# Kernel tuning notes

Hardware: AMD Instinct MI355X
Metric: run time of the kernel (lower is better)

The kernel has to match this reference:

```python
import jax, jax.numpy as jnp
import numpy as np

B_SZ = 1
SEQ = 4096
IN_DIM = 1024
D_MODEL = 512
D_INNER = 1024   # expand(2) * d_model
D_STATE = 16
D_CONV = 4
DT_RANK = 32     # ceil(d_model / 16)
N_LAYERS = 2
N_CLASSES = 2


def setup_inputs() -> dict:
    key = jax.random.key(0)
    ks = jax.random.split(key, 12)
    s = 0.02
    x = jax.random.normal(ks[0], (B_SZ, SEQ, IN_DIM), jnp.float32)
    fc1_w = jax.random.normal(ks[1], (D_MODEL, IN_DIM), jnp.float32) * s
    fc1_b = jnp.zeros((D_MODEL,), jnp.float32)
    ln_w = jnp.ones((N_LAYERS, D_MODEL), jnp.float32)
    ln_b = jnp.zeros((N_LAYERS, D_MODEL), jnp.float32)
    in_proj_w = jax.random.normal(ks[2], (N_LAYERS, 2 * D_INNER, D_MODEL), jnp.float32) * s
    conv_w = jax.random.normal(ks[3], (N_LAYERS, D_INNER, D_CONV), jnp.float32) * 0.1
    conv_b = jnp.zeros((N_LAYERS, D_INNER), jnp.float32)
    x_proj_w = jax.random.normal(ks[4], (N_LAYERS, DT_RANK + 2 * D_STATE, D_INNER), jnp.float32) * s
    dt_proj_w = jax.random.normal(ks[5], (N_LAYERS, D_INNER, DT_RANK), jnp.float32) * s
    # bias so softplus(bias) ~ 0.01 (typical dt init)
    dt_proj_b = jnp.full((N_LAYERS, D_INNER), float(np.log(np.expm1(0.01))), jnp.float32)
    A_log = jnp.broadcast_to(jnp.log(jnp.arange(1, D_STATE + 1, dtype=jnp.float32)),
                             (N_LAYERS, D_INNER, D_STATE)).copy()
    D_skip = jnp.ones((N_LAYERS, D_INNER), jnp.float32)
    norm_w = jnp.ones((D_MODEL,), jnp.float32)
    norm_b = jnp.zeros((D_MODEL,), jnp.float32)
    cls_w = jax.random.normal(ks[6], (N_CLASSES, D_MODEL), jnp.float32) * s
    cls_b = jnp.zeros((N_CLASSES,), jnp.float32)
    return {"x": x, "fc1_w": fc1_w, "fc1_b": fc1_b, "ln_w": ln_w, "ln_b": ln_b,
            "in_proj_w": in_proj_w, "conv_w": conv_w, "conv_b": conv_b,
            "x_proj_w": x_proj_w, "dt_proj_w": dt_proj_w, "dt_proj_b": dt_proj_b,
            "A_log": A_log, "D_skip": D_skip, "norm_w": norm_w, "norm_b": norm_b,
            "cls_w": cls_w, "cls_b": cls_b}


def layernorm(h, w, b, eps=1e-5):
    mu = h.mean(-1, keepdims=True)
    var = ((h - mu) ** 2).mean(-1, keepdims=True)
    return (h - mu) * jax.lax.rsqrt(var + eps) * w + b


def mamba_block(h, in_proj_w, conv_w, conv_b, x_proj_w, dt_proj_w, dt_proj_b, A_log, D_skip):
    # h: [B, L, d_model]
    xz = jnp.einsum('bld,ed->ble', h, in_proj_w)          # [B, L, 2*D_INNER]
    xc, z = jnp.split(xz, 2, axis=-1)                     # each [B, L, D_INNER]
    # causal depthwise conv along L (kernel D_CONV)
    xp = jnp.pad(xc, ((0, 0), (D_CONV - 1, 0), (0, 0)))
    conv = sum(xp[:, k:k + xc.shape[1], :] * conv_w[:, k] for k in range(D_CONV))
    xc = jax.nn.silu(conv + conv_b)
    dbc = jnp.einsum('bld,ed->ble', xc, x_proj_w)         # [B, L, DT_RANK + 2*N]
    dt = jax.nn.softplus(jnp.einsum('blr,dr->bld', dbc[..., :DT_RANK], dt_proj_w) + dt_proj_b)
    Bm = dbc[..., DT_RANK:DT_RANK + D_STATE]              # [B, L, N]
    Cm = dbc[..., DT_RANK + D_STATE:]                     # [B, L, N]
    A = -jnp.exp(A_log)                                   # [D_INNER, N]
    dA = jnp.exp(dt[..., None] * A)                       # [B, L, D_INNER, N]
    dBx = dt[..., None] * Bm[:, :, None, :] * xc[..., None]

    def step(s, ins):
        dA_t, dBx_t, C_t = ins
        s = dA_t * s + dBx_t                              # [B, D_INNER, N]
        y = jnp.einsum('bdn,bn->bd', s, C_t)
        return s, y

    s0 = jnp.zeros((h.shape[0], D_INNER, D_STATE), h.dtype)
    _, ys = jax.lax.scan(step, s0, (dA.transpose(1, 0, 2, 3),
                                    dBx.transpose(1, 0, 2, 3),
                                    Cm.transpose(1, 0, 2)))
    y = ys.transpose(1, 0, 2) + xc * D_skip               # [B, L, D_INNER]
    y = y * jax.nn.silu(z)
    return y


def reference(x, fc1_w, fc1_b, ln_w, ln_b, in_proj_w, conv_w, conv_b,
              x_proj_w, dt_proj_w, dt_proj_b, A_log, D_skip,
              norm_w, norm_b, cls_w, cls_b):
    # out_proj of each Mamba layer folded: out_proj_w stored in in_proj? No -> build here.
    # We use the last N_LAYERS rows trick not needed: out projection is d_inner->d_model,
    # reuse in_proj_w transposed halves would be unfaithful, so derive deterministic weights.
    out_proj_w = jnp.stack([
        jax.random.normal(jax.random.fold_in(jax.random.key(7), i),
                          (D_MODEL, D_INNER), jnp.float32) * 0.02
        for i in range(N_LAYERS)])
    h = jax.nn.gelu(jnp.einsum('bli,di->bld', x, fc1_w) + fc1_b)
    for i in range(N_LAYERS):
        res = h
        hn = layernorm(h, ln_w[i], ln_b[i])
        y = mamba_block(hn, in_proj_w[i], conv_w[i], conv_b[i], x_proj_w[i],
                        dt_proj_w[i], dt_proj_b[i], A_log[i], D_skip[i])
        h = jnp.einsum('ble,de->bld', y, out_proj_w[i]) + res
    h = layernorm(h, norm_w, norm_b)
    hidden = h.mean(axis=1)                               # avg aggregation
    pred = hidden @ cls_w.T + cls_b
    return hidden, pred, h
```

## Files before the change

kernel.cpp:

```cpp
#include <hip/hip_runtime.h>
#include <cstdint>
#include <cstddef>

#define SEQ     4096
#define IN_DIM  1024
#define D_MODEL 512
#define D_INNER 1024
#define D_STATE 16
#define DT_RANK 32

#define CHUNK   32
#define NCHUNK  128
#define NREC    16384

#define LOG2E 1.44269504088896f

static const size_t OFF_H     = 0;
static const size_t OFF_PS    = 2097152;
static const size_t OFF_Z     = 6291456;
static const size_t OFF_XC    = 10485760;
static const size_t OFF_DT    = 14680064;
static const size_t OFF_CARRY = 18874368;
static const size_t OFF_HNB   = 20971520;
static const size_t OFF_FC1WB = 22020096;
static const size_t OFF_WIB   = 22282240;
static const size_t OFF_XPWB  = 23330816;
static const size_t OFF_DPWB  = 23396352;
static const size_t OFF_DBCF  = 23429120;
static const size_t OFF_DBCB  = 23691264;
static const size_t OFF_WOUTB = 23822336;
static const size_t OFF_PART  = 24346624;

typedef __attribute__((ext_vector_type(8))) short bf16x8;
typedef __attribute__((ext_vector_type(4))) float f32x4;

__device__ __forceinline__ uint32_t rotl32(uint32_t v, int r) { return (v << r) | (v >> (32 - r)); }

__device__ __forceinline__ void threefry2x32(uint32_t k0, uint32_t k1, uint32_t x0, uint32_t x1,
                                             uint32_t& o0, uint32_t& o1) {
  uint32_t ks0 = k0, ks1 = k1, ks2 = k0 ^ k1 ^ 0x1BD11BDAu;
  x0 += ks0; x1 += ks1;
  const int rotA[4] = {13, 15, 26, 6};
  const int rotB[4] = {17, 29, 16, 24};
  uint32_t ks[3] = {ks0, ks1, ks2};
#pragma unroll
  for (int r = 0; r < 5; ++r) {
    const int* rr = (r & 1) ? rotB : rotA;
#pragma unroll
    for (int j = 0; j < 4; ++j) { x0 += x1; x1 = rotl32(x1, rr[j]); x1 ^= x0; }
    x0 += ks[(r + 1) % 3];
    x1 += ks[(r + 2) % 3] + (uint32_t)(r + 1);
  }
  o0 = x0; o1 = x1;
}

__device__ __forceinline__ float erfinv32(float x) {
  float w = -log1pf(-x * x);
  float p;
  if (w < 5.0f) {
    w -= 2.5f;
    p = 2.81022636e-08f;
    p = fmaf(p, w, 3.43273939e-07f);
    p = fmaf(p, w, -3.5233877e-06f);
    p = fmaf(p, w, -4.39150654e-06f);
    p = fmaf(p, w, 0.00021858087f);
    p = fmaf(p, w, -0.00125372503f);
    p = fmaf(p, w, -0.00417768164f);
    p = fmaf(p, w, 0.246640727f);
    p = fmaf(p, w, 1.50140941f);
  } else {
    w = sqrtf(w) - 3.0f;
    p = -0.000200214257f;
    p = fmaf(p, w, 0.000100950558f);
    p = fmaf(p, w, 0.00134934322f);
    p = fmaf(p, w, -0.00367342844f);
    p = fmaf(p, w, 0.00573950773f);
    p = fmaf(p, w, -0.0076224613f);
    p = fmaf(p, w, 0.00943887047f);
    p = fmaf(p, w, 1.00167406f);
    p = fmaf(p, w, 2.83297682f);
  }
  return p * x;
}

__device__ __forceinline__ float bits_to_normal(uint32_t b) {
  float f = __uint_as_float((b >> 9) | 0x3f800000u) - 1.0f;
  const float lo = -0.99999994f;
  float u = f * (1.0f - lo) + lo;
  u = fmaxf(lo, u);
  return 1.41421356f * erfinv32(u);
}

__device__ __forceinline__ ushort f2bf(float x) {
  uint32_t u = __float_as_uint(x);
  u = (u + 0x7FFFu + ((u >> 16) & 1u)) >> 16;
  return (ushort)u;
}
__device__ __forceinline__ bf16x8 pack8(float4 a, float4 b) {
  bf16x8 v;
  v[0] = f2bf(a.x); v[1] = f2bf(a.y); v[2] = f2bf(a.z); v[3] = f2bf(a.w);
  v[4] = f2bf(b.x); v[5] = f2bf(b.y); v[6] = f2bf(b.z); v[7] = f2bf(b.w);
  return v;
}

__global__ __launch_bounds__(256) void gen_wout(ushort* __restrict__ w) {
  int gid = blockIdx.x * 256 + threadIdx.x;
  int layer = gid >> 19;
  int j = gid & 0x7FFFF;
  uint32_t k0, k1;
  threefry2x32(0u, 7u, 0u, (uint32_t)layer, k0, k1);
  uint32_t o0, o1;
  threefry2x32(k0, k1, 0u, (uint32_t)j, o0, o1);
  w[(size_t)layer * 524288 + j] = f2bf(bits_to_normal(o0 ^ o1) * 0.02f);
}

__global__ __launch_bounds__(256) void convert_all(
    const float* __restrict__ x,   const float* __restrict__ fc1w,
    const float* __restrict__ ipw, const float* __restrict__ xpw,
    const float* __restrict__ dpw,
    ushort* __restrict__ xb, ushort* __restrict__ fc1wb, ushort* __restrict__ ipwb,
    ushort* __restrict__ xpwb, ushort* __restrict__ dpwb) {
  int gid = blockIdx.x * 256 + threadIdx.x;
  const float* src; ushort* dst; size_t off;
  if (gid < 524288)      { src = x;    dst = xb;    off = gid; }
  else if (gid < 589824) { src = fc1w; dst = fc1wb; off = gid - 524288; }
  else if (gid < 851968) { src = ipw;  dst = ipwb;  off = gid - 589824; }
  else if (gid < 868352) { src = xpw;  dst = xpwb;  off = gid - 851968; }
  else if (gid < 876544) { src = dpw;  dst = dpwb;  off = gid - 868352; }
  else return;
  const float4* p = (const float4*)(src + off * 8);
  *(bf16x8*)(dst + off * 8) = pack8(p[0], p[1]);
}

__device__ __forceinline__ float silu_f(float v) { return v / (1.0f + exp2f(-LOG2E * v)); }
__device__ __forceinline__ float gelu_f(float v) {
  float v3 = v * v * v;
  return 0.5f * v * (1.0f + tanhf(0.7978845608028654f * (v + 0.044715f * v3)));
}
__device__ __forceinline__ float softplus_f(float v) {
  return fmaxf(v, 0.0f) + log1pf(exp2f(-LOG2E * fabsf(v)));
}

enum { EPI_NONE = 0, EPI_BIAS_GELU = 1, EPI_INPROJ = 2, EPI_SOFTPLUS = 3, EPI_RESID = 4, EPI_DBC = 5 };

template <int EPI, int NT>
__global__ __launch_bounds__(256) void gemm_bf(
    const ushort* __restrict__ A, int lda,
    const ushort* __restrict__ B, int ldb,
    float* __restrict__ C, int ldc, int K,
    const float* __restrict__ bias, float* __restrict__ out2,
    ushort* __restrict__ outb) {
  constexpr int NB = NT / 64;
  __shared__ ushort As[2][64][40];
  __shared__ ushort Bs[2][NT][40];
  const int m0 = blockIdx.y * 64, n0 = blockIdx.x * NT;
  const int tid = threadIdx.x;
  const int arow = tid >> 2, ach = (tid & 3) * 8;
  const int lane = tid & 63, wid = tid >> 6;
  const int lr = lane & 15, lhi = lane >> 4;
  const ushort* Ap  = A + (size_t)(m0 + arow) * lda + ach;
  const ushort* Bp0 = B + (size_t)(n0 + arow) * ldb + ach;
  const ushort* Bp1 = (NB > 1) ? (B + (size_t)(n0 + 64 + arow) * ldb + ach) : Bp0;

  f32x4 acc[NT / 16] = {};
  uint4 ra, rb0, rb1;

  ra  = *(const uint4*)Ap;
  rb0 = *(const uint4*)Bp0;
  if (NB > 1) rb1 = *(const uint4*)Bp1;
  *(uint4*)&As[0][arow][ach] = ra;
  *(uint4*)&Bs[0][arow][ach] = rb0;
  if (NB > 1) *(uint4*)&Bs[0][64 + arow][ach] = rb1;
  __syncthreads();

  const int nk = K >> 5;
  int cur = 0;
  for (int ki = 0; ki < nk; ++ki) {
    const bool more = (ki + 1 < nk);
    if (more) {
      const int k = (ki + 1) << 5;
      ra  = *(const uint4*)(Ap + k);
      rb0 = *(const uint4*)(Bp0 + k);
      if (NB > 1) rb1 = *(const uint4*)(Bp1 + k);
    }
    bf16x8 af = *(const bf16x8*)&As[cur][wid * 16 + lr][lhi * 8];
#pragma unroll
    for (int t = 0; t < NT / 16; ++t) {
      bf16x8 bv = *(const bf16x8*)&Bs[cur][t * 16 + lr][lhi * 8];
      acc[t] = __builtin_amdgcn_mfma_f32_16x16x32_bf16(af, bv, acc[t], 0, 0, 0);
    }
    if (more) {
      *(uint4*)&As[cur ^ 1][arow][ach] = ra;
      *(uint4*)&Bs[cur ^ 1][arow][ach] = rb0;
      if (NB > 1) *(uint4*)&Bs[cur ^ 1][64 + arow][ach] = rb1;
    }
    __syncthreads();
    cur ^= 1;
  }

#pragma unroll
  for (int t = 0; t < NT / 16; ++t) {
    const int n = n0 + t * 16 + lr;
#pragma unroll
    for (int r = 0; r < 4; ++r) {
      const int m = m0 + wid * 16 + lhi * 4 + r;
      float v = acc[t][r];
      if (EPI == EPI_NONE) {
        C[(size_t)m * ldc + n] = v;
      } else if (EPI == EPI_BIAS_GELU) {
        v += bias[n];
        C[(size_t)m * ldc + n] = gelu_f(v);
      } else if (EPI == EPI_SOFTPLUS) {
        v += bias[n];
        C[(size_t)m * ldc + n] = softplus_f(v);
      } else if (EPI == EPI_RESID) {
        C[(size_t)m * ldc + n] += v;
      } else if (EPI == EPI_INPROJ) {
        if (n < D_INNER) C[(size_t)m * D_INNER + n] = v;
        else             out2[(size_t)m * D_INNER + (n - D_INNER)] = silu_f(v);
      } else if (EPI == EPI_DBC) {
        C[(size_t)m * 64 + n] = v;
        outb[(size_t)m * 64 + n] = f2bf(v);
      }
    }
  }
}

template <int EPI>
__global__ __launch_bounds__(256) void gemm_bf128(
    const ushort* __restrict__ A, int lda,
    const ushort* __restrict__ B, int ldb,
    float* __restrict__ C, int ldc, int K,
    const float* __restrict__ bias, float* __restrict__ out2) {
  __shared__ ushort As[2][128][40];
  __shared__ ushort Bs[2][128][40];
  const int m0 = blockIdx.y * 128, n0 = blockIdx.x * 128;
  const int tid = threadIdx.x;
  const int lane = tid & 63, wid = tid >> 6;
  const int lr = lane & 15, lhi = lane >> 4;
  const int r0_ = tid >> 2, ach = (tid & 3) * 8;
  const ushort* Ap0 = A + (size_t)(m0 + r0_) * lda + ach;
  const ushort* Ap1 = A + (size_t)(m0 + r0_ + 64) * lda + ach;
  const ushort* Bp0 = B + (size_t)(n0 + r0_) * ldb + ach;
  const ushort* Bp1 = B + (size_t)(n0 + r0_ + 64) * ldb + ach;

  f32x4 acc[16] = {};
  uint4 ra0, ra1, rb0, rb1;

  ra0 = *(const uint4*)Ap0; ra1 = *(const uint4*)Ap1;
  rb0 = *(const uint4*)Bp0; rb1 = *(const uint4*)Bp1;
  *(uint4*)&As[0][r0_][ach] = ra0; *(uint4*)&As[0][r0_ + 64][ach] = ra1;
  *(uint4*)&Bs[0][r0_][ach] = rb0; *(uint4*)&Bs[0][r0_ + 64][ach] = rb1;
  __syncthreads();

  const int nk = K >> 5;
  int cur = 0;
  for (int ki = 0; ki < nk; ++ki) {
    const bool more = (ki + 1 < nk);
    if (more) {
      const int k = (ki + 1) << 5;
      ra0 = *(const uint4*)(Ap0 + k); ra1 = *(const uint4*)(Ap1 + k);
      rb0 = *(const uint4*)(Bp0 + k); rb1 = *(const uint4*)(Bp1 + k);
    }
    bf16x8 af0 = *(const bf16x8*)&As[cur][wid * 32 + lr][lhi * 8];
    bf16x8 af1 = *(const bf16x8*)&As[cur][wid * 32 + 16 + lr][lhi * 8];
#pragma unroll
    for (int t = 0; t < 8; ++t) {
      bf16x8 bv = *(const bf16x8*)&Bs[cur][t * 16 + lr][lhi * 8];
      acc[t]     = __builtin_amdgcn_mfma_f32_16x16x32_bf16(af0, bv, acc[t], 0, 0, 0);
      acc[8 + t] = __builtin_amdgcn_mfma_f32_16x16x32_bf16(af1, bv, acc[8 + t], 0, 0, 0);
    }
    if (more) {
      *(uint4*)&As[cur ^ 1][r0_][ach] = ra0; *(uint4*)&As[cur ^ 1][r0_ + 64][ach] = ra1;
      *(uint4*)&Bs[cur ^ 1][r0_][ach] = rb0; *(uint4*)&Bs[cur ^ 1][r0_ + 64][ach] = rb1;
    }
    __syncthreads();
    cur ^= 1;
  }

#pragma unroll
  for (int fr = 0; fr < 2; ++fr) {
#pragma unroll
    for (int t = 0; t < 8; ++t) {
      const int n = n0 + t * 16 + lr;
#pragma unroll
      for (int r = 0; r < 4; ++r) {
        const int m = m0 + wid * 32 + fr * 16 + lhi * 4 + r;
        float v = acc[fr * 8 + t][r];
        if (EPI == EPI_INPROJ) {
          if (n < D_INNER) C[(size_t)m * D_INNER + n] = v;
          else             out2[(size_t)m * D_INNER + (n - D_INNER)] = silu_f(v);
        } else {
          C[(size_t)m * ldc + n] = v;
        }
      }
    }
  }
}

template <int BF>
__global__ __launch_bounds__(256) void ln_rows(const float* __restrict__ in,
                                               const float* __restrict__ w,
                                               const float* __restrict__ b,
                                               float* __restrict__ outf,
                                               ushort* __restrict__ outb) {
  __shared__ double red[4];
  const int row = blockIdx.x, t = threadIdx.x;
  const float* r = in + (size_t)row * D_MODEL;
  double x0 = (double)r[t], x1 = (double)r[t + 256];
  double s = x0 + x1;
#pragma unroll
  for (int o = 32; o >= 1; o >>= 1) s += __shfl_down(s, o);
  int wid = t >> 6, lane = t & 63;
  if (lane == 0) red[wid] = s;
  __syncthreads();
  double mu = (red[0] + red[1] + red[2] + red[3]) * (1.0 / 512.0);
  __syncthreads();
  double d0 = x0 - mu, d1 = x1 - mu;
  double v = d0 * d0 + d1 * d1;
#pragma unroll
  for (int o = 32; o >= 1; o >>= 1) v += __shfl_down(v, o);
  if (lane == 0) red[wid] = v;
  __syncthreads();
  double var = (red[0] + red[1] + red[2] + red[3]) * (1.0 / 512.0);
  double rs = rsqrt(var + 1e-5);
  float o0 = (float)(d0 * rs * (double)w[t] + (double)b[t]);
  float o1 = (float)(d1 * rs * (double)w[t + 256] + (double)b[t + 256]);
  if (BF) {
    outb[(size_t)row * D_MODEL + t]       = f2bf(o0);
    outb[(size_t)row * D_MODEL + t + 256] = f2bf(o1);
  } else {
    outf[(size_t)row * D_MODEL + t]       = o0;
    outf[(size_t)row * D_MODEL + t + 256] = o1;
  }
}

__global__ __launch_bounds__(256) void conv_silu2(const float* __restrict__ xcr,
                                                  const float* __restrict__ cw,
                                                  const float* __restrict__ cb,
                                                  float* __restrict__ outf,
                                                  ushort* __restrict__ outb) {
  const int l = blockIdx.x;
  for (int q = 0; q < 4; ++q) {
    const int d = threadIdx.x + q * 256;
    float acc = cb[d];
#pragma unroll
    for (int k = 0; k < 4; ++k) {
      const int ll = l + k - 3;
      const float xv = (ll >= 0) ? xcr[(size_t)ll * D_INNER + d] : 0.0f;
      acc = fmaf(xv, cw[d * 4 + k], acc);
    }
    float o = silu_f(acc);
    outf[(size_t)l * D_INNER + d] = o;
    outb[(size_t)l * D_INNER + d] = f2bf(o);
  }
}

__global__ __launch_bounds__(256) void scanA(const float* __restrict__ dt,
                                             const float* __restrict__ dbc,
                                             const float* __restrict__ xc,
                                             const float* __restrict__ Alog,
                                             float* __restrict__ P, float* __restrict__ S) {
  const int c = blockIdx.y;
  const int d = blockIdx.x * 256 + threadIdx.x;
  float a2[16], s[16];
#pragma unroll
  for (int q = 0; q < 4; ++q) {
    float4 al = *(const float4*)(Alog + (size_t)d * 16 + q * 4);
    a2[4*q+0] = -expf(al.x) * LOG2E; a2[4*q+1] = -expf(al.y) * LOG2E;
    a2[4*q+2] = -expf(al.z) * LOG2E; a2[4*q+3] = -expf(al.w) * LOG2E;
  }
#pragma unroll
  for (int n = 0; n < 16; ++n) s[n] = 0.0f;
  float sdt = 0.0f;
  const int l0 = c * CHUNK;
#pragma unroll 2
  for (int t = 0; t < CHUNK; ++t) {
    const int l = l0 + t;
    const float dtv = dt[(size_t)l * D_INNER + d];
    const float xv  = xc[(size_t)l * D_INNER + d];
    const float dx = dtv * xv;
    sdt += dtv;
    float bv[16];
    const float4* B4 = (const float4*)(dbc + (size_t)l * 64 + DT_RANK);
    *(float4*)&bv[0]  = B4[0]; *(float4*)&bv[4]  = B4[1];
    *(float4*)&bv[8]  = B4[2]; *(float4*)&bv[12] = B4[3];
#pragma unroll
    for (int n = 0; n < 16; ++n)
      s[n] = fmaf(exp2f(dtv * a2[n]), s[n], bv[n] * dx);
  }
  float4* Sp = (float4*)(S + (size_t)c * NREC + (size_t)d * 16);
  float4* Pp = (float4*)(P + (size_t)c * NREC + (size_t)d * 16);
#pragma unroll
  for (int q = 0; q < 4; ++q) {
    Sp[q] = make_float4(s[4*q], s[4*q+1], s[4*q+2], s[4*q+3]);
    Pp[q] = make_float4(exp2f(a2[4*q]*sdt), exp2f(a2[4*q+1]*sdt),
                        exp2f(a2[4*q+2]*sdt), exp2f(a2[4*q+3]*sdt));
  }
}

__global__ __launch_bounds__(256) void scanB(const float* __restrict__ P,
                                             const float* __restrict__ S,
                                             float* __restrict__ carry) {
  int idx = blockIdx.x * 256 + threadIdx.x;
  float cr = 0.0f;
  for (int c = 0; c < NCHUNK; ++c) {
    size_t k = (size_t)c * NREC + idx;
    carry[k] = cr;
    cr = fmaf(P[k], cr, S[k]);
  }
}

__global__ __launch_bounds__(256) void scanC(const float* __restrict__ dt,
                                             const float* __restrict__ dbc,
                                             const float* __restrict__ xc,
                                             const float* __restrict__ Alog,
                                             const float* __restrict__ carry,
                                             const float* __restrict__ Dskip,
                                             const float* __restrict__ zs,
                                             ushort* __restrict__ yb) {
  const int c = blockIdx.y;
  const int d = blockIdx.x * 256 + threadIdx.x;
  float a2[16], s[16];
#pragma unroll
  for (int q = 0; q < 4; ++q) {
    float4 al = *(const float4*)(Alog + (size_t)d * 16 + q * 4);
    a2[4*q+0] = -expf(al.x) * LOG2E; a2[4*q+1] = -expf(al.y) * LOG2E;
    a2[4*q+2] = -expf(al.z) * LOG2E; a2[4*q+3] = -expf(al.w) * LOG2E;
    float4 cr = *(const float4*)(carry + (size_t)c * NREC + (size_t)d * 16 + q * 4);
    s[4*q+0] = cr.x; s[4*q+1] = cr.y; s[4*q+2] = cr.z; s[4*q+3] = cr.w;
  }
  const float dsk = Dskip[d];
  const int l0 = c * CHUNK;
#pragma unroll 2
  for (int t = 0; t < CHUNK; ++t) {
    const int l = l0 + t;
    const float dtv = dt[(size_t)l * D_INNER + d];
    const float xv  = xc[(size_t)l * D_INNER + d];
    const float dx = dtv * xv;
    float bv[16], cv[16];
    const float4* B4 = (const float4*)(dbc + (size_t)l * 64 + DT_RANK);
    *(float4*)&bv[0]  = B4[0]; *(float4*)&bv[4]  = B4[1];
    *(float4*)&bv[8]  = B4[2]; *(float4*)&bv[12] = B4[3];
    *(float4*)&cv[0]  = B4[4]; *(float4*)&cv[4]  = B4[5];
    *(float4*)&cv[8]  = B4[6]; *(float4*)&cv[12] = B4[7];
    float acc = 0.0f;
#pragma unroll
    for (int n = 0; n < 16; ++n) {
      s[n] = fmaf(exp2f(dtv * a2[n]), s[n], bv[n] * dx);
      acc = fmaf(s[n], cv[n], acc);
    }
    float yv = fmaf(xv, dsk, acc);
    yb[(size_t)l * D_INNER + d] = f2bf(yv * zs[(size_t)l * D_INNER + d]);
  }
}

__global__ __launch_bounds__(512) void colsum(const float* __restrict__ h, double* __restrict__ part) {
  int d = threadIdx.x;
  int r0 = blockIdx.x * 128;
  double s = 0.0;
  for (int r = 0; r < 128; ++r) s += (double)h[(size_t)(r0 + r) * D_MODEL + d];
  part[blockIdx.x * D_MODEL + d] = s;
}

__global__ __launch_bounds__(512) void head_k(const double* __restrict__ part,
                                              const float* __restrict__ cls_w,
                                              const float* __restrict__ cls_b,
                                              float* __restrict__ out) {
  __shared__ double l0[512], l1[512];
  int d = threadIdx.x;
  double s = 0.0;
  for (int b = 0; b < 32; ++b) s += part[b * D_MODEL + d];
  double hv = s * (1.0 / 4096.0);
  out[d] = (float)hv;
  l0[d] = hv * (double)cls_w[d];
  l1[d] = hv * (double)cls_w[D_MODEL + d];
  __syncthreads();
  for (int o = 256; o > 0; o >>= 1) {
    if (d < o) { l0[d] += l0[d + o]; l1[d] += l1[d + o]; }
    __syncthreads();
  }
  if (d == 0) { out[512] = (float)(l0[0] + (double)cls_b[0]); out[513] = (float)(l1[0] + (double)cls_b[1]); }
}

extern "C" void kernel_launch(void* const* d_in, const int* in_sizes, int n_in,
                              void* d_out, int out_size, void* d_ws, size_t ws_size,
                              hipStream_t stream) {
  const float* x         = (const float*)d_in[0];
  const float* fc1_w     = (const float*)d_in[1];
  const float* fc1_b     = (const float*)d_in[2];
  const float* ln_w      = (const float*)d_in[3];
  const float* ln_b      = (const float*)d_in[4];
  const float* in_proj_w = (const float*)d_in[5];
  const float* conv_w    = (const float*)d_in[6];
  const float* conv_b    = (const float*)d_in[7];
  const float* x_proj_w  = (const float*)d_in[8];
  const float* dt_proj_w = (const float*)d_in[9];
  const float* dt_proj_b = (const float*)d_in[10];
  const float* A_log     = (const float*)d_in[11];
  const float* D_skip    = (const float*)d_in[12];
  const float* norm_w    = (const float*)d_in[13];
  const float* norm_b    = (const float*)d_in[14];
  const float* cls_w     = (const float*)d_in[15];
  const float* cls_b     = (const float*)d_in[16];
  float* out = (float*)d_out;
  float* ws  = (float*)d_ws;

  float*  h_buf   = ws + OFF_H;
  float*  xcraw   = ws + OFF_PS;
  float*  P_buf   = ws + OFF_PS;
  float*  S_buf   = ws + OFF_PS + 2097152;
  ushort* y_bf    = (ushort*)(ws + OFF_PS);
  float*  z_buf   = ws + OFF_Z;
  float*  xc_buf  = ws + OFF_XC;
  float*  dt_buf  = ws + OFF_DT;
  ushort* x_bf    = (ushort*)(ws + OFF_DT);
  ushort* xc_bf   = (ushort*)(ws + OFF_DT);
  float*  carry_b = ws + OFF_CARRY;
  ushort* hn_bf   = (ushort*)(ws + OFF_HNB);
  ushort* fc1w_bf = (ushort*)(ws + OFF_FC1WB);
  ushort* Wi_bf   = (ushort*)(ws + OFF_WIB);
  ushort* xpw_bf  = (ushort*)(ws + OFF_XPWB);
  ushort* dpw_bf  = (ushort*)(ws + OFF_DPWB);
  float*  dbc_f   = ws + OFF_DBCF;
  ushort* dbc_bf  = (ushort*)(ws + OFF_DBCB);
  ushort* wout_bf = (ushort*)(ws + OFF_WOUTB);
  double* part    = (double*)(ws + OFF_PART);

  gen_wout<<<4096, 256, 0, stream>>>(wout_bf);
  convert_all<<<3424, 256, 0, stream>>>(x, fc1_w, in_proj_w, x_proj_w, dt_proj_w,
                                        x_bf, fc1w_bf, Wi_bf, xpw_bf, dpw_bf);

  gemm_bf<EPI_BIAS_GELU, 128><<<dim3(4, 64), 256, 0, stream>>>(
      x_bf, IN_DIM, fc1w_bf, IN_DIM, h_buf, D_MODEL, IN_DIM, fc1_b, nullptr, nullptr);

  for (int i = 0; i < 2; ++i) {
    ln_rows<1><<<4096, 256, 0, stream>>>(h_buf, ln_w + i * D_MODEL, ln_b + i * D_MODEL,
                                         nullptr, hn_bf);
    gemm_bf128<EPI_INPROJ><<<dim3(16, 32), 256, 0, stream>>>(
        hn_bf, D_MODEL, Wi_bf + (size_t)i * 1048576, D_MODEL, xcraw, D_INNER, D_MODEL,
        nullptr, z_buf);
    conv_silu2<<<4096, 256, 0, stream>>>(xcraw, conv_w + (size_t)i * D_INNER * 4,
                                         conv_b + i * D_INNER, xc_buf, xc_bf);
    gemm_bf<EPI_DBC, 64><<<dim3(1, 64), 256, 0, stream>>>(
        xc_bf, D_INNER, xpw_bf + (size_t)i * 65536, D_INNER, dbc_f, 64, D_INNER,
        nullptr, nullptr, dbc_bf);
    gemm_bf<EPI_SOFTPLUS, 128><<<dim3(8, 64), 256, 0, stream>>>(
        dbc_bf, 64, dpw_bf + (size_t)i * 32768, DT_RANK, dt_buf, D_INNER, DT_RANK,
        dt_proj_b + i * D_INNER, nullptr, nullptr);
    const float* Alog_i = A_log + (size_t)i * D_INNER * D_STATE;
    scanA<<<dim3(4, NCHUNK), 256, 0, stream>>>(dt_buf, dbc_f, xc_buf, Alog_i, P_buf, S_buf);
    scanB<<<64, 256, 0, stream>>>(P_buf, S_buf, carry_b);
    scanC<<<dim3(4, NCHUNK), 256, 0, stream>>>(dt_buf, dbc_f, xc_buf, Alog_i, carry_b,
                                               D_skip + i * D_INNER, z_buf, y_bf);
    gemm_bf<EPI_RESID, 128><<<dim3(4, 64), 256, 0, stream>>>(
        y_bf, D_INNER, wout_bf + (size_t)i * 524288, D_INNER, h_buf, D_MODEL, D_INNER,
        nullptr, nullptr, nullptr);
  }

  ln_rows<0><<<4096, 256, 0, stream>>>(h_buf, norm_w, norm_b, out + 514, nullptr);
  colsum<<<32, 512, 0, stream>>>(out + 514, part);
  head_k<<<1, 512, 0, stream>>>(part, cls_w, cls_b, out);
}
```

Baseline: 384.7 us.

## Merge weight-gen/convert kernels, store gate z as bf16, use 128x128 GEMM tiles

Merges the out-projection weight generation and the bf16 conversion into a single launch. Stores the silu gate z as bf16 instead of fp32, halving its write and read traffic in in_proj and scanC. Moves the fc1 and out-projection GEMMs from 64x128 tiles to the 128x128 tile kernel. This halves their block count to 128 workgroups, which may underfill a 256-CU device.

```diff
diff --git a/kernel.cpp b/kernel.cpp
--- a/kernel.cpp
+++ b/kernel.cpp
@@ -96,6 +96,9 @@
   u = (u + 0x7FFFu + ((u >> 16) & 1u)) >> 16;
   return (ushort)u;
 }
+__device__ __forceinline__ float bf2f(ushort u) {
+  return __uint_as_float(((uint32_t)u) << 16);
+}
 __device__ __forceinline__ bf16x8 pack8(float4 a, float4 b) {
   bf16x8 v;
   v[0] = f2bf(a.x); v[1] = f2bf(a.y); v[2] = f2bf(a.z); v[3] = f2bf(a.w);
@@ -103,30 +106,31 @@
   return v;
 }
 
-__global__ __launch_bounds__(256) void gen_wout(ushort* __restrict__ w) {
-  int gid = blockIdx.x * 256 + threadIdx.x;
-  int layer = gid >> 19;
-  int j = gid & 0x7FFFF;
-  uint32_t k0, k1;
-  threefry2x32(0u, 7u, 0u, (uint32_t)layer, k0, k1);
-  uint32_t o0, o1;
-  threefry2x32(k0, k1, 0u, (uint32_t)j, o0, o1);
-  w[(size_t)layer * 524288 + j] = f2bf(bits_to_normal(o0 ^ o1) * 0.02f);
-}
-
-__global__ __launch_bounds__(256) void convert_all(
+__global__ __launch_bounds__(256) void gen_convert(
     const float* __restrict__ x,   const float* __restrict__ fc1w,
     const float* __restrict__ ipw, const float* __restrict__ xpw,
     const float* __restrict__ dpw,
+    ushort* __restrict__ woutb,
     ushort* __restrict__ xb, ushort* __restrict__ fc1wb, ushort* __restrict__ ipwb,
     ushort* __restrict__ xpwb, ushort* __restrict__ dpwb) {
   int gid = blockIdx.x * 256 + threadIdx.x;
+  if (gid < 1048576) {
+    int layer = gid >> 19;
+    int j = gid & 0x7FFFF;
+    uint32_t k0, k1;
+    threefry2x32(0u, 7u, 0u, (uint32_t)layer, k0, k1);
+    uint32_t o0, o1;
+    threefry2x32(k0, k1, 0u, (uint32_t)j, o0, o1);
+    woutb[(size_t)layer * 524288 + j] = f2bf(bits_to_normal(o0 ^ o1) * 0.02f);
+    return;
+  }
+  int g = gid - 1048576;
   const float* src; ushort* dst; size_t off;
-  if (gid < 524288)      { src = x;    dst = xb;    off = gid; }
-  else if (gid < 589824) { src = fc1w; dst = fc1wb; off = gid - 524288; }
-  else if (gid < 851968) { src = ipw;  dst = ipwb;  off = gid - 589824; }
-  else if (gid < 868352) { src = xpw;  dst = xpwb;  off = gid - 851968; }
-  else if (gid < 876544) { src = dpw;  dst = dpwb;  off = gid - 868352; }
+  if (g < 524288)      { src = x;    dst = xb;    off = g; }
+  else if (g < 589824) { src = fc1w; dst = fc1wb; off = g - 524288; }
+  else if (g < 851968) { src = ipw;  dst = ipwb;  off = g - 589824; }
+  else if (g < 868352) { src = xpw;  dst = xpwb;  off = g - 851968; }
+  else if (g < 876544) { src = dpw;  dst = dpwb;  off = g - 868352; }
   else return;
   const float4* p = (const float4*)(src + off * 8);
   *(bf16x8*)(dst + off * 8) = pack8(p[0], p[1]);
@@ -207,17 +211,9 @@
       float v = acc[t][r];
       if (EPI == EPI_NONE) {
         C[(size_t)m * ldc + n] = v;
-      } else if (EPI == EPI_BIAS_GELU) {
-        v += bias[n];
-        C[(size_t)m * ldc + n] = gelu_f(v);
       } else if (EPI == EPI_SOFTPLUS) {
         v += bias[n];
         C[(size_t)m * ldc + n] = softplus_f(v);
-      } else if (EPI == EPI_RESID) {
-        C[(size_t)m * ldc + n] += v;
-      } else if (EPI == EPI_INPROJ) {
-        if (n < D_INNER) C[(size_t)m * D_INNER + n] = v;
-        else             out2[(size_t)m * D_INNER + (n - D_INNER)] = silu_f(v);
       } else if (EPI == EPI_DBC) {
         C[(size_t)m * 64 + n] = v;
         outb[(size_t)m * 64 + n] = f2bf(v);
@@ -231,7 +227,7 @@
     const ushort* __restrict__ A, int lda,
     const ushort* __restrict__ B, int ldb,
     float* __restrict__ C, int ldc, int K,
-    const float* __restrict__ bias, float* __restrict__ out2) {
+    const float* __restrict__ bias, ushort* __restrict__ out2) {
   __shared__ ushort As[2][128][40];
   __shared__ ushort Bs[2][128][40];
   const int m0 = blockIdx.y * 128, n0 = blockIdx.x * 128;
@@ -287,11 +283,14 @@
       for (int r = 0; r < 4; ++r) {
         const int m = m0 + wid * 32 + fr * 16 + lhi * 4 + r;
         float v = acc[fr * 8 + t][r];
-        if (EPI == EPI_INPROJ) {
+        if (EPI == EPI_BIAS_GELU) {
+          v += bias[n];
+          C[(size_t)m * ldc + n] = gelu_f(v);
+        } else if (EPI == EPI_RESID) {
+          C[(size_t)m * ldc + n] += v;
+        } else if (EPI == EPI_INPROJ) {
           if (n < D_INNER) C[(size_t)m * D_INNER + n] = v;
-          else             out2[(size_t)m * D_INNER + (n - D_INNER)] = silu_f(v);
-        } else {
-          C[(size_t)m * ldc + n] = v;
+          else             out2[(size_t)m * D_INNER + (n - D_INNER)] = f2bf(silu_f(v));
         }
       }
     }
@@ -417,7 +416,7 @@
                                              const float* __restrict__ Alog,
                                              const float* __restrict__ carry,
                                              const float* __restrict__ Dskip,
-                                             const float* __restrict__ zs,
+                                             const ushort* __restrict__ zb,
                                              ushort* __restrict__ yb) {
   const int c = blockIdx.y;
   const int d = blockIdx.x * 256 + threadIdx.x;
@@ -451,7 +450,7 @@
       acc = fmaf(s[n], cv[n], acc);
     }
     float yv = fmaf(xv, dsk, acc);
-    yb[(size_t)l * D_INNER + d] = f2bf(yv * zs[(size_t)l * D_INNER + d]);
+    yb[(size_t)l * D_INNER + d] = f2bf(yv * bf2f(zb[(size_t)l * D_INNER + d]));
   }
 }
 
@@ -511,7 +510,7 @@
   float*  P_buf   = ws + OFF_PS;
   float*  S_buf   = ws + OFF_PS + 2097152;
   ushort* y_bf    = (ushort*)(ws + OFF_PS);
-  float*  z_buf   = ws + OFF_Z;
+  ushort* z_bf    = (ushort*)(ws + OFF_Z);
   float*  xc_buf  = ws + OFF_XC;
   float*  dt_buf  = ws + OFF_DT;
   ushort* x_bf    = (ushort*)(ws + OFF_DT);
@@ -527,19 +526,18 @@
   ushort* wout_bf = (ushort*)(ws + OFF_WOUTB);
   double* part    = (double*)(ws + OFF_PART);
 
-  gen_wout<<<4096, 256, 0, stream>>>(wout_bf);
-  convert_all<<<3424, 256, 0, stream>>>(x, fc1_w, in_proj_w, x_proj_w, dt_proj_w,
-                                        x_bf, fc1w_bf, Wi_bf, xpw_bf, dpw_bf);
-
-  gemm_bf<EPI_BIAS_GELU, 128><<<dim3(4, 64), 256, 0, stream>>>(
-      x_bf, IN_DIM, fc1w_bf, IN_DIM, h_buf, D_MODEL, IN_DIM, fc1_b, nullptr, nullptr);
+  gen_convert<<<7520, 256, 0, stream>>>(x, fc1_w, in_proj_w, x_proj_w, dt_proj_w,
+                                        wout_bf, x_bf, fc1w_bf, Wi_bf, xpw_bf, dpw_bf);
+
+  gemm_bf128<EPI_BIAS_GELU><<<dim3(4, 32), 256, 0, stream>>>(
+      x_bf, IN_DIM, fc1w_bf, IN_DIM, h_buf, D_MODEL, IN_DIM, fc1_b, nullptr);
 
   for (int i = 0; i < 2; ++i) {
     ln_rows<1><<<4096, 256, 0, stream>>>(h_buf, ln_w + i * D_MODEL, ln_b + i * D_MODEL,
                                          nullptr, hn_bf);
     gemm_bf128<EPI_INPROJ><<<dim3(16, 32), 256, 0, stream>>>(
         hn_bf, D_MODEL, Wi_bf + (size_t)i * 1048576, D_MODEL, xcraw, D_INNER, D_MODEL,
-        nullptr, z_buf);
+        nullptr, z_bf);
     conv_silu2<<<4096, 256, 0, stream>>>(xcraw, conv_w + (size_t)i * D_INNER * 4,
                                          conv_b + i * D_INNER, xc_buf, xc_bf);
     gemm_bf<EPI_DBC, 64><<<dim3(1, 64), 256, 0, stream>>>(
@@ -552,10 +550,10 @@
     scanA<<<dim3(4, NCHUNK), 256, 0, stream>>>(dt_buf, dbc_f, xc_buf, Alog_i, P_buf, S_buf);
     scanB<<<64, 256, 0, stream>>>(P_buf, S_buf, carry_b);
     scanC<<<dim3(4, NCHUNK), 256, 0, stream>>>(dt_buf, dbc_f, xc_buf, Alog_i, carry_b,
-                                               D_skip + i * D_INNER, z_buf, y_bf);
-    gemm_bf<EPI_RESID, 128><<<dim3(4, 64), 256, 0, stream>>>(
+                                               D_skip + i * D_INNER, z_bf, y_bf);
+    gemm_bf128<EPI_RESID><<<dim3(4, 32), 256, 0, stream>>>(
         y_bf, D_INNER, wout_bf + (size_t)i * 524288, D_INNER, h_buf, D_MODEL, D_INNER,
-        nullptr, nullptr, nullptr);
+        nullptr, nullptr);
   }
 
   ln_rows<0><<<4096, 256, 0, stream>>>(h_buf, norm_w, norm_b, out + 514, nullptr);
```

New measurement: 413.6 us. 1.08x slower.
